# Optimization experiments

Hardware: AMD Instinct MI355X
Metric: run time of the kernel (lower is better)

## Reference

```python
import jax, jax.numpy as jnp
import numpy as np

N = 100000      # nodes
E = 3200000     # edges
NG = 64         # graphs in batch
F_IN, H1, H2 = 128, 128, 64
DENSE = 16 * 8  # first_dense_neurons * second_dense_neurons
LABELS = 2


def setup_inputs() -> dict:
    key = jax.random.key(0)
    ks = jax.random.split(key, 12)
    x = jax.random.normal(ks[0], (N, F_IN), dtype=jnp.float32)
    edge_index = jax.random.randint(ks[1], (2, E), 0, N, dtype=jnp.int32)
    batch = jnp.sort(jax.random.randint(ks[2], (N,), 0, NG, dtype=jnp.int32))
    s = 0.05
    W1 = jax.random.normal(ks[3], (F_IN, H1), dtype=jnp.float32) * s
    b1 = jnp.zeros((H1,), dtype=jnp.float32)
    W2 = jax.random.normal(ks[4], (H1, H2), dtype=jnp.float32) * s
    b2 = jnp.zeros((H2,), dtype=jnp.float32)
    Wf1 = jax.random.normal(ks[5], (H2, DENSE), dtype=jnp.float32) * s
    bf1 = jnp.zeros((DENSE,), dtype=jnp.float32)
    Wf2 = jax.random.normal(ks[6], (DENSE, LABELS), dtype=jnp.float32) * s
    bf2 = jnp.zeros((LABELS,), dtype=jnp.float32)
    return {"x": x, "W1": W1, "b1": b1, "W2": W2, "b2": b2,
            "Wf1": Wf1, "bf1": bf1, "Wf2": Wf2, "bf2": bf2,
            "edge_index": edge_index, "batch": batch}


def _gcn_conv(x, W, b, src, dst, dis):
    # PyG GCNConv: h = x @ W, propagate with sym norm (self-loops included)
    h = x @ W
    coef = (dis[src] * dis[dst])[:, None]          # [E,1]
    agg = jax.ops.segment_sum(h[src] * coef, dst, num_segments=N)
    agg = agg + h * (dis * dis)[:, None]           # self-loop term
    return agg + b


def reference(x, W1, b1, W2, b2, Wf1, bf1, Wf2, bf2, edge_index, batch):
    src, dst = edge_index[0], edge_index[1]
    # degree with self-loops, symmetric normalization D^-1/2 (A+I) D^-1/2
    deg = 1.0 + jax.ops.segment_sum(jnp.ones((E,), x.dtype), dst, num_segments=N)
    dis = jax.lax.rsqrt(deg)
    h1 = jax.nn.relu(_gcn_conv(x, W1, b1, src, dst, dis))
    h2 = jax.nn.relu(_gcn_conv(h1, W2, b2, src, dst, dis))
    a1 = h2 @ Wf1 + bf1                            # [N, DENSE] (dropout: eval mode)
    counts = jax.ops.segment_sum(jnp.ones((N,), x.dtype), batch, num_segments=NG)
    graph_embedding = jax.ops.segment_sum(a1, batch, num_segments=NG) / jnp.maximum(counts, 1.0)[:, None]
    ic_predictions = graph_embedding @ Wf2 + bf2   # [NG, LABELS]
    penalty = jnp.float32(0.0)
    return (graph_embedding, penalty, ic_predictions)
```

## Files before the change

### kernel.cpp

```cpp
#include <hip/hip_runtime.h>


typedef __attribute__((ext_vector_type(8))) short bfrag;
typedef __attribute__((ext_vector_type(16))) float f32x16;
typedef __attribute__((ext_vector_type(2))) float floatx2;

__device__ __forceinline__ unsigned short f2bf(float f) {
    unsigned int u = __builtin_bit_cast(unsigned int, f);
    u = (u + 0x7FFFu + ((u >> 16) & 1u)) >> 16;
    return (unsigned short)u;
}
__device__ __forceinline__ float bf2f(unsigned int lo16) {
    unsigned int v = lo16 << 16;
    return __builtin_bit_cast(float, v);
}
__device__ __forceinline__ unsigned char f2fp8(float f) {
    return (unsigned char)(__builtin_amdgcn_cvt_pk_fp8_f32(f, f, 0, false) & 0xFF);
}
__device__ __forceinline__ void macc8f8(float* acc, const uint2& v, float c) {
    floatx2 f0 = __builtin_amdgcn_cvt_pk_f32_fp8((int)v.x, false);
    floatx2 f1 = __builtin_amdgcn_cvt_pk_f32_fp8((int)v.x, true);
    floatx2 f2 = __builtin_amdgcn_cvt_pk_f32_fp8((int)v.y, false);
    floatx2 f3 = __builtin_amdgcn_cvt_pk_f32_fp8((int)v.y, true);
    acc[0] += f0.x * c; acc[1] += f0.y * c;
    acc[2] += f1.x * c; acc[3] += f1.y * c;
    acc[4] += f2.x * c; acc[5] += f2.y * c;
    acc[6] += f3.x * c; acc[7] += f3.y * c;
}

__global__ __launch_bounds__(256) void bucket_hist_kernel(const int* __restrict__ dst,
                                                          int* __restrict__ bcount, int E) {
    __shared__ int h[256];
    int t = threadIdx.x;
    h[t] = 0;
    __syncthreads();
    int base = blockIdx.x * 4096;
#pragma unroll
    for (int i = 0; i < 16; ++i) {
        int e = base + t + i * 256;
        if (e < E) atomicAdd(&h[dst[e] >> 9], 1);
    }
    __syncthreads();
    if (h[t] > 0) atomicAdd(&bcount[t], h[t]);
}

__global__ void bucket_scan_kernel(const int* __restrict__ bcount, int* __restrict__ bstart,
                                   int* __restrict__ rowstart, int NB, int N, int E) {
    __shared__ int s[256];
    int t = threadIdx.x;
    int v = (t < NB) ? bcount[t] : 0;
    s[t] = v;
    __syncthreads();
    for (int off = 1; off < 256; off <<= 1) {
        int tmp = 0;
        if (t >= off) tmp = s[t - off];
        __syncthreads();
        s[t] += tmp;
        __syncthreads();
    }
    bstart[t] = s[t] - v;
    if (t == 255) bstart[256] = s[255];
    if (t == 0) rowstart[N] = E;
}

__global__ __launch_bounds__(256) void bucket_scatter_kernel(const int* __restrict__ src,
                                                             const int* __restrict__ dst,
                                                             const int* __restrict__ bstart,
                                                             int* __restrict__ bfill,
                                                             unsigned int* __restrict__ stage,
                                                             int E) {
    __shared__ int hist[256];
    __shared__ int abase[256];
    int t = threadIdx.x;
    hist[t] = 0;
    __syncthreads();
    int base = blockIdx.x * 4096;
#pragma unroll
    for (int i = 0; i < 16; ++i) {
        int e = base + t + i * 256;
        if (e < E) atomicAdd(&hist[dst[e] >> 9], 1);
    }
    __syncthreads();
    if (hist[t] > 0) {
        int r = atomicAdd(&bfill[t], hist[t]);
        abase[t] = bstart[t] + r;
    }
    __syncthreads();
    hist[t] = 0;
    __syncthreads();
#pragma unroll
    for (int i = 0; i < 16; ++i) {
        int e = base + t + i * 256;
        if (e < E) {
            int d = dst[e];
            int b = d >> 9;
            int slot = atomicAdd(&hist[b], 1);
            stage[abase[b] + slot] = (unsigned)src[e] | ((unsigned)(d & 511) << 17);
        }
    }
}

__global__ __launch_bounds__(256) void csr_build_kernel(const unsigned int* __restrict__ stage,
                                                        const int* __restrict__ bstart,
                                                        int* __restrict__ rowstart,
                                                        float* __restrict__ dis,
                                                        int* __restrict__ csr_src, int N) {
    __shared__ int cnt[512];
    __shared__ int ofs[512];
    __shared__ int psum[256];
    int b = blockIdx.x, t = threadIdx.x;
    int node0 = b << 9;
    int nb = min(512, N - node0);
    cnt[t] = 0;
    cnt[t + 256] = 0;
    __syncthreads();
    int eb = bstart[b], ee = bstart[b + 1];
    for (int e = eb + t; e < ee; e += 256) {
        unsigned w = stage[e];
        atomicAdd(&cnt[w >> 17], 1);
    }
    __syncthreads();
    int a = cnt[2 * t], c = cnt[2 * t + 1];
    int ps = a + c;
    psum[t] = ps;
    __syncthreads();
    for (int off = 1; off < 256; off <<= 1) {
        int tmp = 0;
        if (t >= off) tmp = psum[t - off];
        __syncthreads();
        psum[t] += tmp;
        __syncthreads();
    }
    int ex = psum[t] - ps;
    ofs[2 * t] = ex;
    ofs[2 * t + 1] = ex + a;
    if (2 * t < nb) {
        rowstart[node0 + 2 * t] = eb + ex;
        dis[node0 + 2 * t] = rsqrtf(1.f + (float)a);
    }
    if (2 * t + 1 < nb) {
        rowstart[node0 + 2 * t + 1] = eb + ex + a;
        dis[node0 + 2 * t + 1] = rsqrtf(1.f + (float)c);
    }
    __syncthreads();
    for (int e = eb + t; e < ee; e += 256) {
        unsigned w = stage[e];
        int l = w >> 17;
        int slot = atomicAdd(&ofs[l], 1);
        csr_src[eb + slot] = (int)(w & 0x1FFFFu);
    }
}

template <int K, int NC>
__global__ __launch_bounds__(256) void wprep_kernel(const float* __restrict__ W,
                                                    unsigned short* __restrict__ Wf) {
    constexpr int CT = NC / 32, KT = K / 16;
    int idx = blockIdx.x * blockDim.x + threadIdx.x;
    if (idx >= KT * CT * 64) return;
    int l = idx & 63;
    int fi = idx >> 6;
    int ct = fi % CT, kt = fi / CT;
    int n = ct * 32 + (l & 31);
    int k0 = kt * 16 + 8 * (l >> 5);
    unsigned short v[8];
#pragma unroll
    for (int j = 0; j < 8; ++j) v[j] = f2bf(W[(size_t)(k0 + j) * NC + n]);
    uint4 o;
    o.x = (unsigned)v[0] | ((unsigned)v[1] << 16);
    o.y = (unsigned)v[2] | ((unsigned)v[3] << 16);
    o.z = (unsigned)v[4] | ((unsigned)v[5] << 16);
    o.w = (unsigned)v[6] | ((unsigned)v[7] << 16);
    *(uint4*)&Wf[(size_t)idx * 8] = o;
}

template <int K, int NC, bool IN_F32>
__global__ __launch_bounds__(256) void gemm_mfma_kernel(const void* __restrict__ Av,
                                                        const unsigned short* __restrict__ Wf,
                                                        unsigned char* __restrict__ C,
                                                        int M) {
    constexpr int KT = K / 16, CT = NC / 32;
    int wid = (blockIdx.x * blockDim.x + threadIdx.x) >> 6;
    int lane = threadIdx.x & 63;
    int row0 = wid * 32;
    if (row0 >= M) return;

    bfrag B[KT][CT];
#pragma unroll
    for (int kt = 0; kt < KT; ++kt)
#pragma unroll
        for (int ct = 0; ct < CT; ++ct)
            B[kt][ct] = *(const bfrag*)&Wf[(size_t)((kt * CT + ct) * 64 + lane) * 8];

    f32x16 acc[CT];
#pragma unroll
    for (int ct = 0; ct < CT; ++ct)
#pragma unroll
        for (int i = 0; i < 16; ++i) acc[ct][i] = 0.f;

    int r = row0 + (lane & 31);
    if (r >= M) r = M - 1;
#pragma unroll
    for (int kt = 0; kt < KT; ++kt) {
        bfrag a;
        if (IN_F32) {
            const float* Arow = &((const float*)Av)[(size_t)r * K + 8 * (lane >> 5)];
            float4 v0 = *(const float4*)&Arow[kt * 16];
            float4 v1 = *(const float4*)&Arow[kt * 16 + 4];
            a[0] = (short)f2bf(v0.x); a[1] = (short)f2bf(v0.y);
            a[2] = (short)f2bf(v0.z); a[3] = (short)f2bf(v0.w);
            a[4] = (short)f2bf(v1.x); a[5] = (short)f2bf(v1.y);
            a[6] = (short)f2bf(v1.z); a[7] = (short)f2bf(v1.w);
        } else {
            const unsigned short* Arow =
                &((const unsigned short*)Av)[(size_t)r * K + 8 * (lane >> 5)];
            a = *(const bfrag*)&Arow[kt * 16];
        }
#pragma unroll
        for (int ct = 0; ct < CT; ++ct)
            acc[ct] = __builtin_amdgcn_mfma_f32_32x32x16_bf16(a, B[kt][ct], acc[ct], 0, 0, 0);
    }

    int colb = lane & 31;
    int rowq = 4 * (lane >> 5);
#pragma unroll
    for (int ct = 0; ct < CT; ++ct) {
        int col = ct * 32 + colb;
#pragma unroll
        for (int rg = 0; rg < 16; ++rg) {
            int row = row0 + (rg & 3) + 8 * (rg >> 2) + rowq;
            if (row < M) C[(size_t)row * NC + col] = f2fp8(acc[ct][rg]);
        }
    }
}

template <int NC>
__global__ __launch_bounds__(256) void aggregate_kernel(const unsigned char* __restrict__ h,
                                                        const float* __restrict__ dis,
                                                        const int* __restrict__ rowstart,
                                                        const int* __restrict__ csr_src,
                                                        const float* __restrict__ bias,
                                                        unsigned short* __restrict__ out,
                                                        int N) {
    constexpr int LPR = NC / 8;
    constexpr int RPS = 64 / LPR;
    int wid = (blockIdx.x * blockDim.x + threadIdx.x) >> 6;
    int lane = threadIdx.x & 63;
    if (wid >= N) return;
    int n = wid;
    int sub = lane / LPR;
    int fid = lane % LPR;
    const uint2* h8 = (const uint2*)h;
    float d = dis[n];
    float acc[8];
#pragma unroll
    for (int i = 0; i < 8; ++i) acc[i] = 0.f;
    if (sub == 0) {
        uint2 hv = h8[(size_t)n * LPR + fid];
        macc8f8(acc, hv, d);
    }

    int beg = rowstart[n], end = rowstart[n + 1];
    for (int e0 = beg; e0 < end; e0 += 64) {
        int idx = e0 + lane;
        int sv = 0;
        float dv = 0.f;
        if (idx < end) { sv = csr_src[idx]; dv = dis[sv]; }
        int cnt = min(64, end - e0);
        int j = 0;
        for (; j + 2 * RPS <= cnt; j += 2 * RPS) {
            int ja = j + sub, jb = j + RPS + sub;
            int sa = __shfl(sv, ja); float ca = __shfl(dv, ja);
            int sb = __shfl(sv, jb); float cb = __shfl(dv, jb);
            uint2 va = h8[(size_t)sa * LPR + fid];
            uint2 vb = h8[(size_t)sb * LPR + fid];
            macc8f8(acc, va, ca);
            macc8f8(acc, vb, cb);
        }
        for (; j < cnt; j += RPS) {
            int jj = j + sub;
            int jc = min(jj, cnt - 1);
            int s = __shfl(sv, jc);
            float c = __shfl(dv, jc);
            if (jj >= cnt) c = 0.f;
            uint2 v = h8[(size_t)s * LPR + fid];
            macc8f8(acc, v, c);
        }
    }
#pragma unroll
    for (int m = LPR; m < 64; m <<= 1) {
#pragma unroll
        for (int i = 0; i < 8; ++i) acc[i] += __shfl_xor(acc[i], m);
    }
    if (sub == 0) {
        const float4 bv0 = *(const float4*)&bias[fid * 8 + 0];
        const float4 bv1 = *(const float4*)&bias[fid * 8 + 4];
        float r[8];
        r[0] = fmaxf(acc[0] * d + bv0.x, 0.f);
        r[1] = fmaxf(acc[1] * d + bv0.y, 0.f);
        r[2] = fmaxf(acc[2] * d + bv0.z, 0.f);
        r[3] = fmaxf(acc[3] * d + bv0.w, 0.f);
        r[4] = fmaxf(acc[4] * d + bv1.x, 0.f);
        r[5] = fmaxf(acc[5] * d + bv1.y, 0.f);
        r[6] = fmaxf(acc[6] * d + bv1.z, 0.f);
        r[7] = fmaxf(acc[7] * d + bv1.w, 0.f);
        uint4 o;
        o.x = (unsigned)f2bf(r[0]) | ((unsigned)f2bf(r[1]) << 16);
        o.y = (unsigned)f2bf(r[2]) | ((unsigned)f2bf(r[3]) << 16);
        o.z = (unsigned)f2bf(r[4]) | ((unsigned)f2bf(r[5]) << 16);
        o.w = (unsigned)f2bf(r[6]) | ((unsigned)f2bf(r[7]) << 16);
        *(uint4*)&out[(size_t)n * NC + fid * 8] = o;
    }
}

__global__ __launch_bounds__(64) void pool_kernel(const unsigned short* __restrict__ h2,
                                                  const int* __restrict__ batch,
                                                  float* __restrict__ gsum, int N) {
    int f = threadIdx.x;
    int n0 = blockIdx.x * 128;
    int nend = min(n0 + 128, N);
    float acc = 0.f;
    int gcur = batch[n0];
    for (int n = n0; n < nend; ++n) {
        int g = batch[n];
        if (g != gcur) {
            atomicAdd(&gsum[gcur * 64 + f], acc);
            acc = 0.f;
            gcur = g;
        }
        acc += bf2f(h2[(size_t)n * 64 + f]);
    }
    atomicAdd(&gsum[gcur * 64 + f], acc);
}

__global__ __launch_bounds__(256) void count_batch_kernel(const int* __restrict__ batch,
                                                          int* __restrict__ gcnt, int N) {
    __shared__ int lc[64];
    int t = threadIdx.x;
    if (t < 64) lc[t] = 0;
    __syncthreads();
    int n = blockIdx.x * blockDim.x + t;
    if (n < N) atomicAdd(&lc[batch[n]], 1);
    __syncthreads();
    if (t < 64 && lc[t] > 0) atomicAdd(&gcnt[t], lc[t]);
}

__global__ __launch_bounds__(128) void head_kernel(const float* __restrict__ gsum,
                                                   const int* __restrict__ gcnt,
                                                   const float* __restrict__ Wf1,
                                                   const float* __restrict__ bf1,
                                                   const float* __restrict__ Wf2,
                                                   const float* __restrict__ bf2,
                                                   float* __restrict__ out) {
    __shared__ float ph[64];
    __shared__ float red0[128], red1[128];
    int g = blockIdx.x, f = threadIdx.x;
    if (f < 64) ph[f] = gsum[g * 64 + f] / (float)max(gcnt[g], 1);
    __syncthreads();
    float ge = bf1[f];
#pragma unroll 8
    for (int k = 0; k < 64; ++k) ge += ph[k] * Wf1[k * 128 + f];
    out[g * 128 + f] = ge;
    red0[f] = ge * Wf2[f * 2 + 0];
    red1[f] = ge * Wf2[f * 2 + 1];
    __syncthreads();
    for (int off = 64; off > 0; off >>= 1) {
        if (f < off) { red0[f] += red0[f + off]; red1[f] += red1[f + off]; }
        __syncthreads();
    }
    if (f == 0) {
        out[8192 + 1 + g * 2 + 0] = red0[0] + bf2[0];
        out[8192 + 1 + g * 2 + 1] = red1[0] + bf2[1];
        if (g == 0) out[8192] = 0.f;
    }
}

extern "C" void kernel_launch(void* const* d_in, const int* in_sizes, int n_in,
                              void* d_out, int out_size, void* d_ws, size_t ws_size,
                              hipStream_t stream) {
    const float* x   = (const float*)d_in[0];
    const float* W1  = (const float*)d_in[1];
    const float* b1  = (const float*)d_in[2];
    const float* W2  = (const float*)d_in[3];
    const float* b2  = (const float*)d_in[4];
    const float* Wf1 = (const float*)d_in[5];
    const float* bf1 = (const float*)d_in[6];
    const float* Wf2 = (const float*)d_in[7];
    const float* bf2 = (const float*)d_in[8];
    const int* edge  = (const int*)d_in[9];
    const int* batch = (const int*)d_in[10];

    const int N = in_sizes[10];
    const int E = in_sizes[9] / 2;
    const int* srcA = edge;
    const int* dstA = edge + E;
    float* out = (float*)d_out;

    const int NB = (N + 511) >> 9;

    char* p = (char*)d_ws;
    auto alloc = [&](size_t bytes) {
        char* r = p;
        p += (bytes + 255) & ~(size_t)255;
        return r;
    };
    float* gsum     = (float*)alloc(64 * 64 * 4);
    int*   gcnt     = (int*)alloc(64 * 4);
    int*   bcount   = (int*)alloc(256 * 4);
    int*   bfill    = (int*)alloc(256 * 4);
    size_t zbytes   = (size_t)(p - (char*)d_ws);
    int*   bstart   = (int*)alloc(260 * 4);
    float* dis      = (float*)alloc((size_t)N * 4);
    int*   rowstart = (int*)alloc((size_t)(N + 1) * 4);
    unsigned short* Wp1 = (unsigned short*)alloc(8 * 4 * 64 * 8 * 2);
    unsigned short* Wp2 = (unsigned short*)alloc(8 * 2 * 64 * 8 * 2);
    unsigned int* stage = (unsigned int*)alloc((size_t)E * 4);
    int*   csr_src  = (int*)alloc((size_t)E * 4);
    unsigned char*  hf8   = (unsigned char*)alloc((size_t)N * 128);
    unsigned short* h1b   = (unsigned short*)alloc((size_t)N * 128 * 2);
    unsigned short* h2b   = (unsigned short*)alloc((size_t)N * 64 * 2);

    hipMemsetAsync(d_ws, 0, zbytes, stream);

    const int EB = (E + 4095) / 4096;
    bucket_hist_kernel<<<EB, 256, 0, stream>>>(dstA, bcount, E);
    bucket_scan_kernel<<<1, 256, 0, stream>>>(bcount, bstart, rowstart, NB, N, E);
    bucket_scatter_kernel<<<EB, 256, 0, stream>>>(srcA, dstA, bstart, bfill, stage, E);
    csr_build_kernel<<<NB, 256, 0, stream>>>(stage, bstart, rowstart, dis, csr_src, N);

    wprep_kernel<128, 128><<<8, 256, 0, stream>>>(W1, Wp1);
    wprep_kernel<128, 64><<<4, 256, 0, stream>>>(W2, Wp2);

    const int GB = (N + 127) / 128;
    gemm_mfma_kernel<128, 128, true><<<GB, 256, 0, stream>>>(x, Wp1, hf8, N);
    aggregate_kernel<128><<<(N + 3) / 4, 256, 0, stream>>>(hf8, dis, rowstart, csr_src,
                                                           b1, h1b, N);
    gemm_mfma_kernel<128, 64, false><<<GB, 256, 0, stream>>>(h1b, Wp2, hf8, N);
    aggregate_kernel<64><<<(N + 3) / 4, 256, 0, stream>>>(hf8, dis, rowstart, csr_src,
                                                          b2, h2b, N);
    pool_kernel<<<(N + 127) / 128, 64, 0, stream>>>(h2b, batch, gsum, N);
    count_batch_kernel<<<(N + 255) / 256, 256, 0, stream>>>(batch, gcnt, N);
    head_kernel<<<64, 128, 0, stream>>>(gsum, gcnt, Wf1, bf1, Wf2, bf2, out);
}
```

Before: 434.5 us.

## Split GCN aggregation into 32-column passes over column-blocked fp8 features

The GEMM now writes fp8 features in a column-blocked layout with 32-column panels stored contiguously per node. Aggregation launches one grid pass per panel, so each gather touches a smaller working set (N*32 bytes) that fits better in cache, at the cost of re-reading the CSR indices and dis values once per pass. The CSR index loads and the output stores are also marked nontemporal. The change trades extra index traffic and more sequential passes for better locality of the random feature gathers.

```diff
diff --git a/kernel.cpp b/kernel.cpp
--- a/kernel.cpp
+++ b/kernel.cpp
@@ -4,6 +4,7 @@
 typedef __attribute__((ext_vector_type(8))) short bfrag;
 typedef __attribute__((ext_vector_type(16))) float f32x16;
 typedef __attribute__((ext_vector_type(2))) float floatx2;
+typedef __attribute__((ext_vector_type(4))) unsigned int uint32x4;
 
 __device__ __forceinline__ unsigned short f2bf(float f) {
     unsigned int u = __builtin_bit_cast(unsigned int, f);
@@ -224,11 +225,10 @@
     int rowq = 4 * (lane >> 5);
 #pragma unroll
     for (int ct = 0; ct < CT; ++ct) {
-        int col = ct * 32 + colb;
 #pragma unroll
         for (int rg = 0; rg < 16; ++rg) {
             int row = row0 + (rg & 3) + 8 * (rg >> 2) + rowq;
-            if (row < M) C[(size_t)row * NC + col] = f2fp8(acc[ct][rg]);
+            if (row < M) C[((size_t)ct * M + row) * 32 + colb] = f2fp8(acc[ct][rg]);
         }
     }
 }
@@ -241,21 +241,22 @@
                                                         const float* __restrict__ bias,
                                                         unsigned short* __restrict__ out,
                                                         int N) {
-    constexpr int LPR = NC / 8;
+    constexpr int LPR = 4;
     constexpr int RPS = 64 / LPR;
     int wid = (blockIdx.x * blockDim.x + threadIdx.x) >> 6;
     int lane = threadIdx.x & 63;
+    int pass = blockIdx.y;
     if (wid >= N) return;
     int n = wid;
-    int sub = lane / LPR;
-    int fid = lane % LPR;
-    const uint2* h8 = (const uint2*)h;
+    int sub = lane >> 2;
+    int fid = lane & 3;
+    const uint2* h8 = (const uint2*)h + (size_t)pass * N * 4;
     float d = dis[n];
     float acc[8];
 #pragma unroll
     for (int i = 0; i < 8; ++i) acc[i] = 0.f;
     if (sub == 0) {
-        uint2 hv = h8[(size_t)n * LPR + fid];
+        uint2 hv = h8[(size_t)n * 4 + fid];
         macc8f8(acc, hv, d);
     }
 
@@ -264,15 +265,18 @@
         int idx = e0 + lane;
         int sv = 0;
         float dv = 0.f;
-        if (idx < end) { sv = csr_src[idx]; dv = dis[sv]; }
+        if (idx < end) {
+            sv = __builtin_nontemporal_load(&csr_src[idx]);
+            dv = dis[sv];
+        }
         int cnt = min(64, end - e0);
         int j = 0;
         for (; j + 2 * RPS <= cnt; j += 2 * RPS) {
             int ja = j + sub, jb = j + RPS + sub;
             int sa = __shfl(sv, ja); float ca = __shfl(dv, ja);
             int sb = __shfl(sv, jb); float cb = __shfl(dv, jb);
-            uint2 va = h8[(size_t)sa * LPR + fid];
-            uint2 vb = h8[(size_t)sb * LPR + fid];
+            uint2 va = h8[(size_t)sa * 4 + fid];
+            uint2 vb = h8[(size_t)sb * 4 + fid];
             macc8f8(acc, va, ca);
             macc8f8(acc, vb, cb);
         }
@@ -282,7 +286,7 @@
             int s = __shfl(sv, jc);
             float c = __shfl(dv, jc);
             if (jj >= cnt) c = 0.f;
-            uint2 v = h8[(size_t)s * LPR + fid];
+            uint2 v = h8[(size_t)s * 4 + fid];
             macc8f8(acc, v, c);
         }
     }
@@ -292,8 +296,8 @@
         for (int i = 0; i < 8; ++i) acc[i] += __shfl_xor(acc[i], m);
     }
     if (sub == 0) {
-        const float4 bv0 = *(const float4*)&bias[fid * 8 + 0];
-        const float4 bv1 = *(const float4*)&bias[fid * 8 + 4];
+        const float4 bv0 = *(const float4*)&bias[pass * 32 + fid * 8 + 0];
+        const float4 bv1 = *(const float4*)&bias[pass * 32 + fid * 8 + 4];
         float r[8];
         r[0] = fmaxf(acc[0] * d + bv0.x, 0.f);
         r[1] = fmaxf(acc[1] * d + bv0.y, 0.f);
@@ -303,12 +307,12 @@
         r[5] = fmaxf(acc[5] * d + bv1.y, 0.f);
         r[6] = fmaxf(acc[6] * d + bv1.z, 0.f);
         r[7] = fmaxf(acc[7] * d + bv1.w, 0.f);
-        uint4 o;
+        uint32x4 o;
         o.x = (unsigned)f2bf(r[0]) | ((unsigned)f2bf(r[1]) << 16);
         o.y = (unsigned)f2bf(r[2]) | ((unsigned)f2bf(r[3]) << 16);
         o.z = (unsigned)f2bf(r[4]) | ((unsigned)f2bf(r[5]) << 16);
         o.w = (unsigned)f2bf(r[6]) | ((unsigned)f2bf(r[7]) << 16);
-        *(uint4*)&out[(size_t)n * NC + fid * 8] = o;
+        __builtin_nontemporal_store(o, (uint32x4*)&out[(size_t)n * NC + pass * 32 + fid * 8]);
     }
 }
 
@@ -432,11 +436,11 @@
 
     const int GB = (N + 127) / 128;
     gemm_mfma_kernel<128, 128, true><<<GB, 256, 0, stream>>>(x, Wp1, hf8, N);
-    aggregate_kernel<128><<<(N + 3) / 4, 256, 0, stream>>>(hf8, dis, rowstart, csr_src,
-                                                           b1, h1b, N);
+    aggregate_kernel<128><<<dim3((N + 3) / 4, 4), 256, 0, stream>>>(hf8, dis, rowstart,
+                                                                    csr_src, b1, h1b, N);
     gemm_mfma_kernel<128, 64, false><<<GB, 256, 0, stream>>>(h1b, Wp2, hf8, N);
-    aggregate_kernel<64><<<(N + 3) / 4, 256, 0, stream>>>(hf8, dis, rowstart, csr_src,
-                                                          b2, h2b, N);
+    aggregate_kernel<64><<<dim3((N + 3) / 4, 2), 256, 0, stream>>>(hf8, dis, rowstart,
+                                                                   csr_src, b2, h2b, N);
     pool_kernel<<<(N + 127) / 128, 64, 0, stream>>>(h2b, batch, gsum, N);
     count_batch_kernel<<<(N + 255) / 256, 256, 0, stream>>>(batch, gcnt, N);
     head_kernel<<<64, 128, 0, stream>>>(gsum, gcnt, Wf1, bf1, Wf2, bf2, out);
```

New measurement: 629.8 us. +45.0%, slower.

## Precompute per-edge source norms and load edges directly in aggregation

Applied to the files above, without the earlier changes.

Adds a kernel that expands dis[csr_src] into a per-edge csr_dis array, reusing the stage buffer, so both aggregation passes read contiguous coefficients instead of doing a dependent random gather. The aggregation loop now has each lane group load its own edge index and coefficient with nontemporal loads, replacing the 64-wide load plus shuffle broadcast. It also uses packed float2 multiply-accumulate and shift-based row addressing. The cost is an extra pass over E edges plus extra memory traffic for csr_dis, and redundant index loads across lanes within a row.

```diff
diff --git a/kernel.cpp b/kernel.cpp
--- a/kernel.cpp
+++ b/kernel.cpp
@@ -17,15 +17,12 @@
 __device__ __forceinline__ unsigned char f2fp8(float f) {
     return (unsigned char)(__builtin_amdgcn_cvt_pk_fp8_f32(f, f, 0, false) & 0xFF);
 }
-__device__ __forceinline__ void macc8f8(float* acc, const uint2& v, float c) {
-    floatx2 f0 = __builtin_amdgcn_cvt_pk_f32_fp8((int)v.x, false);
-    floatx2 f1 = __builtin_amdgcn_cvt_pk_f32_fp8((int)v.x, true);
-    floatx2 f2 = __builtin_amdgcn_cvt_pk_f32_fp8((int)v.y, false);
-    floatx2 f3 = __builtin_amdgcn_cvt_pk_f32_fp8((int)v.y, true);
-    acc[0] += f0.x * c; acc[1] += f0.y * c;
-    acc[2] += f1.x * c; acc[3] += f1.y * c;
-    acc[4] += f2.x * c; acc[5] += f2.y * c;
-    acc[6] += f3.x * c; acc[7] += f3.y * c;
+__device__ __forceinline__ void macc8v(floatx2* a, const uint2 v, float c) {
+    floatx2 cc = {c, c};
+    a[0] += __builtin_amdgcn_cvt_pk_f32_fp8((int)v.x, false) * cc;
+    a[1] += __builtin_amdgcn_cvt_pk_f32_fp8((int)v.x, true) * cc;
+    a[2] += __builtin_amdgcn_cvt_pk_f32_fp8((int)v.y, false) * cc;
+    a[3] += __builtin_amdgcn_cvt_pk_f32_fp8((int)v.y, true) * cc;
 }
 
 __global__ __launch_bounds__(256) void bucket_hist_kernel(const int* __restrict__ dst,
@@ -148,6 +145,17 @@
         int l = w >> 17;
         int slot = atomicAdd(&ofs[l], 1);
         csr_src[eb + slot] = (int)(w & 0x1FFFFu);
+    }
+}
+
+__global__ __launch_bounds__(256) void csr_expand_kernel(const int* __restrict__ csr_src,
+                                                         const float* __restrict__ dis,
+                                                         float* __restrict__ csr_dis, int E) {
+    int i = blockIdx.x * 1024 + threadIdx.x;
+#pragma unroll
+    for (int k = 0; k < 4; ++k) {
+        int e = i + k * 256;
+        if (e < E) csr_dis[e] = dis[csr_src[e]];
     }
 }
 
@@ -238,71 +246,70 @@
                                                         const float* __restrict__ dis,
                                                         const int* __restrict__ rowstart,
                                                         const int* __restrict__ csr_src,
+                                                        const float* __restrict__ csr_dis,
                                                         const float* __restrict__ bias,
                                                         unsigned short* __restrict__ out,
                                                         int N) {
     constexpr int LPR = NC / 8;
     constexpr int RPS = 64 / LPR;
+    constexpr int SH = (NC == 128) ? 7 : 6;
     int wid = (blockIdx.x * blockDim.x + threadIdx.x) >> 6;
     int lane = threadIdx.x & 63;
     if (wid >= N) return;
     int n = wid;
     int sub = lane / LPR;
     int fid = lane % LPR;
-    const uint2* h8 = (const uint2*)h;
+    unsigned fb = (unsigned)(fid << 3);
     float d = dis[n];
-    float acc[8];
-#pragma unroll
-    for (int i = 0; i < 8; ++i) acc[i] = 0.f;
+    floatx2 acc2[4];
+#pragma unroll
+    for (int i = 0; i < 4; ++i) acc2[i] = (floatx2){0.f, 0.f};
     if (sub == 0) {
-        uint2 hv = h8[(size_t)n * LPR + fid];
-        macc8f8(acc, hv, d);
+        uint2 hv = *(const uint2*)(h + (((unsigned)n << SH) | fb));
+        macc8v(acc2, hv, d);
     }
 
     int beg = rowstart[n], end = rowstart[n + 1];
-    for (int e0 = beg; e0 < end; e0 += 64) {
-        int idx = e0 + lane;
-        int sv = 0;
-        float dv = 0.f;
-        if (idx < end) { sv = csr_src[idx]; dv = dis[sv]; }
-        int cnt = min(64, end - e0);
-        int j = 0;
-        for (; j + 2 * RPS <= cnt; j += 2 * RPS) {
-            int ja = j + sub, jb = j + RPS + sub;
-            int sa = __shfl(sv, ja); float ca = __shfl(dv, ja);
-            int sb = __shfl(sv, jb); float cb = __shfl(dv, jb);
-            uint2 va = h8[(size_t)sa * LPR + fid];
-            uint2 vb = h8[(size_t)sb * LPR + fid];
-            macc8f8(acc, va, ca);
-            macc8f8(acc, vb, cb);
+    int e = beg;
+    for (; e + 2 * RPS <= end; e += 2 * RPS) {
+        int   s0 = __builtin_nontemporal_load(&csr_src[e + sub]);
+        float c0 = __builtin_nontemporal_load(&csr_dis[e + sub]);
+        int   s1 = __builtin_nontemporal_load(&csr_src[e + RPS + sub]);
+        float c1 = __builtin_nontemporal_load(&csr_dis[e + RPS + sub]);
+        uint2 v0 = *(const uint2*)(h + (((unsigned)s0 << SH) | fb));
+        uint2 v1 = *(const uint2*)(h + (((unsigned)s1 << SH) | fb));
+        macc8v(acc2, v0, c0);
+        macc8v(acc2, v1, c1);
+    }
+    for (; e < end; e += RPS) {
+        int idx = e + sub;
+        bool ok = idx < end;
+        int ii = ok ? idx : beg;
+        int s = csr_src[ii];
+        float c = ok ? csr_dis[ii] : 0.f;
+        uint2 v = *(const uint2*)(h + (((unsigned)s << SH) | fb));
+        macc8v(acc2, v, c);
+    }
+#pragma unroll
+    for (int m = LPR; m < 64; m <<= 1) {
+#pragma unroll
+        for (int i = 0; i < 4; ++i) {
+            acc2[i].x += __shfl_xor(acc2[i].x, m);
+            acc2[i].y += __shfl_xor(acc2[i].y, m);
         }
-        for (; j < cnt; j += RPS) {
-            int jj = j + sub;
-            int jc = min(jj, cnt - 1);
-            int s = __shfl(sv, jc);
-            float c = __shfl(dv, jc);
-            if (jj >= cnt) c = 0.f;
-            uint2 v = h8[(size_t)s * LPR + fid];
-            macc8f8(acc, v, c);
-        }
-    }
-#pragma unroll
-    for (int m = LPR; m < 64; m <<= 1) {
-#pragma unroll
-        for (int i = 0; i < 8; ++i) acc[i] += __shfl_xor(acc[i], m);
     }
     if (sub == 0) {
         const float4 bv0 = *(const float4*)&bias[fid * 8 + 0];
         const float4 bv1 = *(const float4*)&bias[fid * 8 + 4];
         float r[8];
-        r[0] = fmaxf(acc[0] * d + bv0.x, 0.f);
-        r[1] = fmaxf(acc[1] * d + bv0.y, 0.f);
-        r[2] = fmaxf(acc[2] * d + bv0.z, 0.f);
-        r[3] = fmaxf(acc[3] * d + bv0.w, 0.f);
-        r[4] = fmaxf(acc[4] * d + bv1.x, 0.f);
-        r[5] = fmaxf(acc[5] * d + bv1.y, 0.f);
-        r[6] = fmaxf(acc[6] * d + bv1.z, 0.f);
-        r[7] = fmaxf(acc[7] * d + bv1.w, 0.f);
+        r[0] = fmaxf(acc2[0].x * d + bv0.x, 0.f);
+        r[1] = fmaxf(acc2[0].y * d + bv0.y, 0.f);
+        r[2] = fmaxf(acc2[1].x * d + bv0.z, 0.f);
+        r[3] = fmaxf(acc2[1].y * d + bv0.w, 0.f);
+        r[4] = fmaxf(acc2[2].x * d + bv1.x, 0.f);
+        r[5] = fmaxf(acc2[2].y * d + bv1.y, 0.f);
+        r[6] = fmaxf(acc2[3].x * d + bv1.z, 0.f);
+        r[7] = fmaxf(acc2[3].y * d + bv1.w, 0.f);
         uint4 o;
         o.x = (unsigned)f2bf(r[0]) | ((unsigned)f2bf(r[1]) << 16);
         o.y = (unsigned)f2bf(r[2]) | ((unsigned)f2bf(r[3]) << 16);
@@ -418,6 +425,7 @@
     unsigned char*  hf8   = (unsigned char*)alloc((size_t)N * 128);
     unsigned short* h1b   = (unsigned short*)alloc((size_t)N * 128 * 2);
     unsigned short* h2b   = (unsigned short*)alloc((size_t)N * 64 * 2);
+    float* csr_dis  = (float*)stage;
 
     hipMemsetAsync(d_ws, 0, zbytes, stream);
 
@@ -426,6 +434,7 @@
     bucket_scan_kernel<<<1, 256, 0, stream>>>(bcount, bstart, rowstart, NB, N, E);
     bucket_scatter_kernel<<<EB, 256, 0, stream>>>(srcA, dstA, bstart, bfill, stage, E);
     csr_build_kernel<<<NB, 256, 0, stream>>>(stage, bstart, rowstart, dis, csr_src, N);
+    csr_expand_kernel<<<(E + 1023) / 1024, 256, 0, stream>>>(csr_src, dis, csr_dis, E);
 
     wprep_kernel<128, 128><<<8, 256, 0, stream>>>(W1, Wp1);
     wprep_kernel<128, 64><<<4, 256, 0, stream>>>(W2, Wp2);
@@ -433,10 +442,10 @@
     const int GB = (N + 127) / 128;
     gemm_mfma_kernel<128, 128, true><<<GB, 256, 0, stream>>>(x, Wp1, hf8, N);
     aggregate_kernel<128><<<(N + 3) / 4, 256, 0, stream>>>(hf8, dis, rowstart, csr_src,
-                                                           b1, h1b, N);
+                                                           csr_dis, b1, h1b, N);
     gemm_mfma_kernel<128, 64, false><<<GB, 256, 0, stream>>>(h1b, Wp2, hf8, N);
     aggregate_kernel<64><<<(N + 3) / 4, 256, 0, stream>>>(hf8, dis, rowstart, csr_src,
-                                                          b2, h2b, N);
+                                                          csr_dis, b2, h2b, N);
     pool_kernel<<<(N + 127) / 128, 64, 0, stream>>>(h2b, batch, gsum, N);
     count_batch_kernel<<<(N + 255) / 256, 256, 0, stream>>>(batch, gcnt, N);
     head_kernel<<<64, 128, 0, stream>>>(gsum, gcnt, Wf1, bf1, Wf2, bf2, out);
```

New measurement: 495.7 us. 1.14x slower.
